# Kernel tuning notes

Measured on AMD Instinct MI355X. Metric: run time of the kernel, lower is better.

## Reference

```python
import jax, jax.numpy as jnp
import numpy as np

B, N_AIM, N_DET, C = 4, 2048, 2048, 256  # inplanes=256, inter_channels=128


def _lin(x, w, b):
    # torch nn.Linear: y = x @ W^T + b, weight shape [out, in]
    return jnp.einsum('bnc,dc->bnd', x, w) + b


def setup_inputs() -> dict:
    key = jax.random.key(0)
    ks = jax.random.split(key, 16)
    s = 1.0 / np.sqrt(C)
    inp = {
        'detect': jax.random.normal(ks[0], (B, N_DET, C), jnp.float32),
        'aim': jax.random.normal(ks[1], (B, N_AIM, C), jnp.float32),
    }
    names = ['g', 'g2', 'theta', 'phi', 'W', 'Q']
    for i, nm in enumerate(names):
        inp[nm + '_w'] = jax.random.uniform(ks[2 + 2 * i], (C, C), jnp.float32, -s, s)
        inp[nm + '_b'] = jax.random.uniform(ks[3 + 2 * i], (C,), jnp.float32, -s, s)
    return inp


def reference(detect, aim, g_w, g_b, g2_w, g2_b, theta_w, theta_b, phi_w, phi_b, W_w, W_b, Q_w, Q_b):
    b, na, c = aim.shape
    nd = detect.shape[1]
    ic = c // 2  # inter_channels

    # view(B, ic, -1) on a contiguous [B, N, C] tensor -> row-major reshape to [B, ic, 2N]
    d_x = _lin(detect, g_w, g_b).reshape(b, ic, -1).transpose(0, 2, 1)      # (B, 2Nd, ic)
    a_x = _lin(aim, g2_w, g2_b).reshape(b, ic, -1).transpose(0, 2, 1)       # (B, 2Na, ic)
    theta_x = _lin(aim, theta_w, theta_b).reshape(b, ic, -1).transpose(0, 2, 1)  # (B, 2Na, ic)
    phi_x = _lin(detect, phi_w, phi_b).reshape(b, ic, -1)                   # (B, ic, 2Nd)

    f = jnp.matmul(theta_x, phi_x)                 # (B, 2Na, 2Nd)
    f_div_C = f / f.shape[-1]                      # scale by 2*Nd
    fi_div_C = jnp.swapaxes(f, 1, 2) / f.shape[-2] # (B, 2Nd, 2Na), scale by 2*Na

    non_aim = jnp.matmul(f_div_C, d_x)             # (B, 2Na, ic)
    non_aim = non_aim.transpose(0, 2, 1).reshape(b, na, c)
    non_aim = _lin(non_aim, W_w, W_b) + aim

    non_det = jnp.matmul(fi_div_C, a_x)            # (B, 2Nd, ic)
    non_det = non_det.transpose(0, 2, 1).reshape(b, nd, c)
    non_det = _lin(non_det, Q_w, Q_b) + detect

    return (non_det, non_aim)
```

## Files before the change

kernel.cpp:

```cpp
#include <hip/hip_runtime.h>


typedef __attribute__((ext_vector_type(4))) float  f32x4;
typedef __attribute__((ext_vector_type(8))) __bf16 bf16x8;
typedef __attribute__((ext_vector_type(8))) unsigned short u16x8;
typedef __attribute__((ext_vector_type(4))) unsigned short u16x4;

__device__ inline unsigned short f2bf(float f) {
    union { float f; unsigned u; } c; c.f = f;
    unsigned r = c.u + 0x7FFF + ((c.u >> 16) & 1);
    return (unsigned short)(r >> 16);
}
__device__ inline bf16x8 ldfrag(const unsigned short* p) {
    return __builtin_bit_cast(bf16x8, *(const u16x8*)p);
}

__global__ __launch_bounds__(256)
void prep_kernel(const float* __restrict__ g_w, const float* __restrict__ g2_w,
                 const float* __restrict__ th_w, const float* __restrict__ ph_w,
                 const float* __restrict__ W_w, const float* __restrict__ Q_w,
                 const float* __restrict__ aim, const float* __restrict__ detect,
                 unsigned short* __restrict__ dst)
{
    const int z = blockIdx.y;
    const float* src; size_t n4; unsigned short* o;
    if (z == 0)      { src = g_w;    n4 = 16384;  o = dst; }
    else if (z == 1) { src = g2_w;   n4 = 16384;  o = dst + 65536; }
    else if (z == 2) { src = th_w;   n4 = 16384;  o = dst + 2 * 65536; }
    else if (z == 3) { src = ph_w;   n4 = 16384;  o = dst + 3 * 65536; }
    else if (z == 4) { src = W_w;    n4 = 16384;  o = dst + 4 * 65536; }
    else if (z == 5) { src = Q_w;    n4 = 16384;  o = dst + 5 * 65536; }
    else if (z == 6) { src = aim;    n4 = 524288; o = dst + 6 * 65536; }
    else             { src = detect; n4 = 524288; o = dst + 6 * 65536 + 2097152; }
    const size_t stride = (size_t)gridDim.x * 256;
    for (size_t i = blockIdx.x * 256 + threadIdx.x; i < n4; i += stride) {
        float4 v = ((const float4*)src)[i];
        u16x4 p; p[0]=f2bf(v.x); p[1]=f2bf(v.y); p[2]=f2bf(v.z); p[3]=f2bf(v.w);
        ((u16x4*)o)[i] = p;
    }
}

__global__ __launch_bounds__(256)
void lin4_kernel(const unsigned short* __restrict__ Abf, const unsigned short* __restrict__ Dbf,
                 const unsigned short* __restrict__ Wb,
                 const float* __restrict__ b_g, const float* __restrict__ b_g2,
                 const float* __restrict__ b_th, const float* __restrict__ b_ph,
                 unsigned short* __restrict__ T,  unsigned short* __restrict__ Ga,
                 unsigned short* __restrict__ P,  unsigned short* __restrict__ Gd)
{
    const int z = blockIdx.z, set = blockIdx.x;
    const unsigned short* A = z ? Dbf : Abf;
    const int wslot = z ? (set ? 0 : 3) : (set ? 1 : 2);
    const unsigned short* Wm = Wb + (size_t)wslot * 65536;
    const float* Bv = z ? (set ? b_g : b_ph) : (set ? b_g2 : b_th);
    unsigned short* O = z ? (set ? Gd : P) : (set ? Ga : T);
    const int m0 = blockIdx.y * 64;

    __shared__ unsigned short As[64][40];
    __shared__ unsigned short Bs[256][40];

    const int tid = threadIdx.x, lane = tid & 63, w = tid >> 6;
    const int wr = w >> 1, wc = w & 1, q = lane >> 4, ln = lane & 15;

    f32x4 acc[2][8] = {};

    for (int k0 = 0; k0 < 256; k0 += 32) {
        {
            int row = tid >> 2, c8 = tid & 3;
            *(u16x8*)&As[row][c8 * 8] = *(const u16x8*)(A + (size_t)(m0 + row) * 256 + k0 + c8 * 8);
        }
        #pragma unroll
        for (int i = 0; i < 4; ++i) {
            int c = tid + i * 256, row = c >> 2, c8 = c & 3;
            *(u16x8*)&Bs[row][c8 * 8] = *(const u16x8*)(Wm + (size_t)row * 256 + k0 + c8 * 8);
        }
        __syncthreads();
        bf16x8 af[2], bb[8];
        #pragma unroll
        for (int i = 0; i < 2; ++i) af[i] = ldfrag(&As[wr * 32 + i * 16 + ln][q * 8]);
        #pragma unroll
        for (int j = 0; j < 8; ++j) bb[j] = ldfrag(&Bs[wc * 128 + j * 16 + ln][q * 8]);
        #pragma unroll
        for (int i = 0; i < 2; ++i)
            #pragma unroll
            for (int j = 0; j < 8; ++j)
                acc[i][j] = __builtin_amdgcn_mfma_f32_16x16x32_bf16(af[i], bb[j], acc[i][j], 0, 0, 0);
        __syncthreads();
    }

    #pragma unroll
    for (int i = 0; i < 2; ++i)
        #pragma unroll
        for (int j = 0; j < 8; ++j) {
            int n = wc * 128 + j * 16 + ln;
            float bias = Bv[n];
            #pragma unroll
            for (int r = 0; r < 4; ++r) {
                int m = m0 + wr * 32 + i * 16 + q * 4 + r;
                O[(size_t)m * 256 + n] = f2bf(acc[i][j][r] + bias);
            }
        }
}

__global__ __launch_bounds__(256)
void s_part_kernel(const unsigned short* __restrict__ Gd, const unsigned short* __restrict__ P,
                   const unsigned short* __restrict__ Ga, const unsigned short* __restrict__ T,
                   float* __restrict__ Spart)
{
    const int bz = blockIdx.x;
    const int which = bz >> 7, rem = bz & 127, batch = rem >> 5, chunk = rem & 31;
    const unsigned short* A = (which ? Ga : Gd) + (size_t)batch * 524288;
    const unsigned short* B = (which ? T  : P ) + (size_t)batch * 524288;
    float* out = Spart + ((size_t)(which * 4 + batch) * 32 + chunk) * 16384;
    const int kbeg = chunk * 128;

    __shared__ unsigned short As[128][72], Bs[128][72];
    const int tid = threadIdx.x, lane = tid & 63, w = tid >> 6;
    const int wr = w >> 1, wc = w & 1, q = lane >> 4, ln = lane & 15;

    f32x4 acc[4][4] = {};

    for (int kk = 0; kk < 2; ++kk) {
        const int k0 = kbeg + kk * 64;
        #pragma unroll
        for (int i = 0; i < 4; ++i) {
            int c = tid + i * 256, row = c >> 3, c8 = c & 7;
            *(u16x8*)&As[row][c8 * 8] = *(const u16x8*)(A + (size_t)row * 4096 + k0 + c8 * 8);
            *(u16x8*)&Bs[row][c8 * 8] = *(const u16x8*)(B + (size_t)row * 4096 + k0 + c8 * 8);
        }
        __syncthreads();
        #pragma unroll
        for (int ks = 0; ks < 2; ++ks) {
            bf16x8 af[4], bb[4];
            #pragma unroll
            for (int i = 0; i < 4; ++i) af[i] = ldfrag(&As[wr * 64 + i * 16 + ln][ks * 32 + q * 8]);
            #pragma unroll
            for (int j = 0; j < 4; ++j) bb[j] = ldfrag(&Bs[wc * 64 + j * 16 + ln][ks * 32 + q * 8]);
            #pragma unroll
            for (int i = 0; i < 4; ++i)
                #pragma unroll
                for (int j = 0; j < 4; ++j)
                    acc[i][j] = __builtin_amdgcn_mfma_f32_16x16x32_bf16(af[i], bb[j], acc[i][j], 0, 0, 0);
        }
        __syncthreads();
    }

    #pragma unroll
    for (int i = 0; i < 4; ++i)
        #pragma unroll
        for (int j = 0; j < 4; ++j)
            #pragma unroll
            for (int r = 0; r < 4; ++r) {
                int m = wr * 64 + i * 16 + q * 4 + r, n = wc * 64 + j * 16 + ln;
                out[m * 128 + n] = acc[i][j][r];
            }
}

__global__ __launch_bounds__(256)
void sred_kernel(const float* __restrict__ Spart, float* __restrict__ S)
{
    const int idx = blockIdx.x * 256 + threadIdx.x;
    const int c = idx >> 14, e = idx & 16383;
    float s = 0.f;
    #pragma unroll
    for (int k = 0; k < 32; ++k) s += Spart[((size_t)(c * 32 + k) << 14) + e];
    S[idx] = s;
}

__global__ __launch_bounds__(256)
void nand_kernel(const float* __restrict__ S,
                 const unsigned short* __restrict__ T, const unsigned short* __restrict__ P,
                 unsigned short* __restrict__ NA, unsigned short* __restrict__ ND)
{
    const int which = blockIdx.z >> 2, batch = blockIdx.z & 3;
    const float* Sm = S + (size_t)(which * 4 + batch) * 16384;
    const unsigned short* Bsrc = (which ? P : T) + (size_t)batch * 524288;
    unsigned short* O = (which ? ND : NA) + (size_t)batch * 524288;
    const int j0 = blockIdx.x * 64;

    __shared__ unsigned short As[128][136];
    __shared__ unsigned short Bs[64][136];

    const int tid = threadIdx.x, lane = tid & 63, w = tid >> 6;
    const int wr = w >> 1, wc = w & 1, q = lane >> 4, ln = lane & 15;

    #pragma unroll
    for (int i = 0; i < 16; ++i) {
        int c = tid + i * 256, row = c >> 5, c4 = c & 31;
        float4 v = *((const float4*)(Sm + (size_t)row * 128) + c4);
        u16x4 p; p[0]=f2bf(v.x); p[1]=f2bf(v.y); p[2]=f2bf(v.z); p[3]=f2bf(v.w);
        *(u16x4*)&As[row][c4 * 4] = p;
    }
    #pragma unroll
    for (int i = 0; i < 4; ++i) {
        int c = tid + i * 256, k = c >> 3, jj0 = (c & 7) * 8;
        u16x8 v = *(const u16x8*)(Bsrc + (size_t)k * 4096 + j0 + jj0);
        #pragma unroll
        for (int jj = 0; jj < 8; ++jj) Bs[jj0 + jj][k] = v[jj];
    }
    __syncthreads();

    f32x4 acc[4][2] = {};
    #pragma unroll
    for (int ks = 0; ks < 4; ++ks) {
        bf16x8 af[4], bb[2];
        #pragma unroll
        for (int i = 0; i < 4; ++i) af[i] = ldfrag(&As[wr * 64 + i * 16 + ln][ks * 32 + q * 8]);
        #pragma unroll
        for (int j = 0; j < 2; ++j) bb[j] = ldfrag(&Bs[wc * 32 + j * 16 + ln][ks * 32 + q * 8]);
        #pragma unroll
        for (int i = 0; i < 4; ++i)
            #pragma unroll
            for (int j = 0; j < 2; ++j)
                acc[i][j] = __builtin_amdgcn_mfma_f32_16x16x32_bf16(af[i], bb[j], acc[i][j], 0, 0, 0);
    }

    #pragma unroll
    for (int i = 0; i < 4; ++i)
        #pragma unroll
        for (int j = 0; j < 2; ++j)
            #pragma unroll
            for (int r = 0; r < 4; ++r) {
                int m = wr * 64 + i * 16 + q * 4 + r;
                int jj = j0 + wc * 32 + j * 16 + ln;
                O[(size_t)m * 4096 + jj] = f2bf(acc[i][j][r] * (1.0f / 4096.0f));
            }
}

__global__ __launch_bounds__(256)
void final_kernel(const unsigned short* __restrict__ NA, const unsigned short* __restrict__ ND,
                  const unsigned short* __restrict__ Wb,
                  const float* __restrict__ W_b, const float* __restrict__ Q_b,
                  const float* __restrict__ aim, const float* __restrict__ detect,
                  float* __restrict__ out_aim, float* __restrict__ out_det)
{
    const int z = blockIdx.z;
    const unsigned short* A = z ? ND : NA;
    const unsigned short* Wm = Wb + (size_t)(z ? 5 : 4) * 65536;
    const float* Bv = z ? Q_b : W_b;
    const float* R  = z ? detect : aim;
    float* O = z ? out_det : out_aim;
    const int m0 = blockIdx.y * 64, n0 = blockIdx.x * 128;

    __shared__ unsigned short As[64][40], Bs[128][40];
    const int tid = threadIdx.x, lane = tid & 63, w = tid >> 6;
    const int wr = w >> 1, wc = w & 1, q = lane >> 4, ln = lane & 15;

    f32x4 acc[2][4] = {};

    for (int k0 = 0; k0 < 256; k0 += 32) {
        {
            int row = tid >> 2, c8 = tid & 3;
            *(u16x8*)&As[row][c8 * 8] = *(const u16x8*)(A + (size_t)(m0 + row) * 256 + k0 + c8 * 8);
        }
        #pragma unroll
        for (int i = 0; i < 2; ++i) {
            int c = tid + i * 256, row = c >> 2, c8 = c & 3;
            *(u16x8*)&Bs[row][c8 * 8] = *(const u16x8*)(Wm + (size_t)(n0 + row) * 256 + k0 + c8 * 8);
        }
        __syncthreads();
        bf16x8 af[2], bb[4];
        #pragma unroll
        for (int i = 0; i < 2; ++i) af[i] = ldfrag(&As[wr * 32 + i * 16 + ln][q * 8]);
        #pragma unroll
        for (int j = 0; j < 4; ++j) bb[j] = ldfrag(&Bs[wc * 64 + j * 16 + ln][q * 8]);
        #pragma unroll
        for (int i = 0; i < 2; ++i)
            #pragma unroll
            for (int j = 0; j < 4; ++j)
                acc[i][j] = __builtin_amdgcn_mfma_f32_16x16x32_bf16(af[i], bb[j], acc[i][j], 0, 0, 0);
        __syncthreads();
    }

    #pragma unroll
    for (int i = 0; i < 2; ++i)
        #pragma unroll
        for (int j = 0; j < 4; ++j) {
            int n = n0 + wc * 64 + j * 16 + ln;
            float bias = Bv[n];
            #pragma unroll
            for (int r = 0; r < 4; ++r) {
                int m = m0 + wr * 32 + i * 16 + q * 4 + r;
                O[(size_t)m * 256 + n] = acc[i][j][r] + bias + R[(size_t)m * 256 + n];
            }
        }
}

extern "C" void kernel_launch(void* const* d_in, const int* in_sizes, int n_in,
                              void* d_out, int out_size, void* d_ws, size_t ws_size,
                              hipStream_t stream)
{
    const float* detect = (const float*)d_in[0];
    const float* aim    = (const float*)d_in[1];
    const float* g_w  = (const float*)d_in[2];  const float* g_b  = (const float*)d_in[3];
    const float* g2_w = (const float*)d_in[4];  const float* g2_b = (const float*)d_in[5];
    const float* th_w = (const float*)d_in[6];  const float* th_b = (const float*)d_in[7];
    const float* ph_w = (const float*)d_in[8];  const float* ph_b = (const float*)d_in[9];
    const float* W_w  = (const float*)d_in[10]; const float* W_b  = (const float*)d_in[11];
    const float* Q_w  = (const float*)d_in[12]; const float* Q_b  = (const float*)d_in[13];

    const size_t TOT = 8192L * 256;

    unsigned short* ws16 = (unsigned short*)d_ws;
    unsigned short* Wbf = ws16;
    unsigned short* Abf = Wbf + 6 * 65536;
    unsigned short* Dbf = Abf + TOT;
    unsigned short* T   = Dbf + TOT;
    unsigned short* P   = T  + TOT;
    unsigned short* Gd  = P  + TOT;
    unsigned short* Ga  = Gd + TOT;
    unsigned short* NA  = Ga + TOT;
    unsigned short* ND  = NA + TOT;
    float* S     = (float*)(ND + TOT);
    float* Spart = S + 2 * 4 * 16384;

    float* out_det = (float*)d_out;
    float* out_aim = out_det + TOT;

    prep_kernel<<<dim3(256, 8), 256, 0, stream>>>(
        g_w, g2_w, th_w, ph_w, W_w, Q_w, aim, detect, Wbf);
    lin4_kernel<<<dim3(2, 128, 2), 256, 0, stream>>>(
        Abf, Dbf, Wbf, g_b, g2_b, th_b, ph_b, T, Ga, P, Gd);
    s_part_kernel<<<dim3(256), 256, 0, stream>>>(Gd, P, Ga, T, Spart);
    sred_kernel<<<dim3(512), 256, 0, stream>>>(Spart, S);
    nand_kernel<<<dim3(64, 1, 8), 256, 0, stream>>>(S, T, P, NA, ND);
    final_kernel<<<dim3(2, 128, 2), 256, 0, stream>>>(
        NA, ND, Wbf, W_b, Q_b, aim, detect, out_aim, out_det);
}
```

Baseline: 137.9 us.

## Fuse all stages into one cooperative persistent kernel with grid syncs

```diff
diff --git a/kernel.cpp b/kernel.cpp
--- a/kernel.cpp
+++ b/kernel.cpp
@@ -1,4 +1,7 @@
 #include <hip/hip_runtime.h>
+#include <hip/hip_cooperative_groups.h>
+
+namespace cg = cooperative_groups;
 
 
 typedef __attribute__((ext_vector_type(4))) float  f32x4;
@@ -15,55 +18,294 @@
     return __builtin_bit_cast(bf16x8, *(const u16x8*)p);
 }
 
+struct Params {
+    const float *detect, *aim;
+    const float *g_w, *g2_w, *th_w, *ph_w, *W_w, *Q_w;
+    const float *g_b, *g2_b, *th_b, *ph_b, *W_b, *Q_b;
+    unsigned short *Wbf, *Abf, *Dbf, *T, *P, *Gd, *Ga, *NA, *ND;
+    float *S, *Spart;
+    float *out_det, *out_aim;
+};
+
+__global__ __launch_bounds__(256, 2)
+void mega_kernel(Params p)
+{
+    cg::grid_group grid = cg::this_grid();
+    const int bx = blockIdx.x, tid = threadIdx.x;
+    const int lane = tid & 63, w = tid >> 6;
+    const int wr = w >> 1, wc = w & 1, q = lane >> 4, ln = lane & 15;
+
+    __shared__ union {
+        struct { unsigned short As[64][40];  unsigned short Bs[256][40]; } lin;
+        struct { unsigned short As[128][40]; unsigned short Bs[128][40]; } sp;
+        struct { unsigned short As[128][72]; unsigned short Bs[64][72];  } nd;
+        struct { unsigned short As[64][40];  unsigned short Bs[128][40]; } fin;
+    } sm;
+
+    {
+        const int z = bx >> 6, sub = bx & 63;
+        const float* src; size_t n4; unsigned short* o;
+        switch (z) {
+            case 0: src = p.g_w;    n4 = 16384;  o = p.Wbf;             break;
+            case 1: src = p.g2_w;   n4 = 16384;  o = p.Wbf + 65536;     break;
+            case 2: src = p.th_w;   n4 = 16384;  o = p.Wbf + 2*65536;   break;
+            case 3: src = p.ph_w;   n4 = 16384;  o = p.Wbf + 3*65536;   break;
+            case 4: src = p.W_w;    n4 = 16384;  o = p.Wbf + 4*65536;   break;
+            case 5: src = p.Q_w;    n4 = 16384;  o = p.Wbf + 5*65536;   break;
+            case 6: src = p.aim;    n4 = 524288; o = p.Abf;             break;
+            default:src = p.detect; n4 = 524288; o = p.Dbf;             break;
+        }
+        for (size_t i = (size_t)sub * 256 + tid; i < n4; i += 64 * 256) {
+            float4 v = ((const float4*)src)[i];
+            u16x4 pk; pk[0]=f2bf(v.x); pk[1]=f2bf(v.y); pk[2]=f2bf(v.z); pk[3]=f2bf(v.w);
+            ((u16x4*)o)[i] = pk;
+        }
+    }
+    grid.sync();
+
+    {
+        const int set = bx & 1, z = (bx >> 1) & 1;
+        const int m0 = (bx >> 2) * 64;
+        const unsigned short* A = z ? p.Dbf : p.Abf;
+        const int wslot = z ? (set ? 0 : 3) : (set ? 1 : 2);
+        const unsigned short* Wm = p.Wbf + (size_t)wslot * 65536;
+        const float* Bv = z ? (set ? p.g_b : p.ph_b) : (set ? p.g2_b : p.th_b);
+        unsigned short* O = z ? (set ? p.Gd : p.P) : (set ? p.Ga : p.T);
+
+        f32x4 acc[2][8] = {};
+        for (int k0 = 0; k0 < 256; k0 += 32) {
+            {
+                int row = tid >> 2, c8 = tid & 3;
+                *(u16x8*)&sm.lin.As[row][c8 * 8] =
+                    *(const u16x8*)(A + (size_t)(m0 + row) * 256 + k0 + c8 * 8);
+            }
+            #pragma unroll
+            for (int i = 0; i < 4; ++i) {
+                int c = tid + i * 256, row = c >> 2, c8 = c & 3;
+                *(u16x8*)&sm.lin.Bs[row][c8 * 8] =
+                    *(const u16x8*)(Wm + (size_t)row * 256 + k0 + c8 * 8);
+            }
+            __syncthreads();
+            bf16x8 af[2], bb[8];
+            #pragma unroll
+            for (int i = 0; i < 2; ++i) af[i] = ldfrag(&sm.lin.As[wr * 32 + i * 16 + ln][q * 8]);
+            #pragma unroll
+            for (int j = 0; j < 8; ++j) bb[j] = ldfrag(&sm.lin.Bs[wc * 128 + j * 16 + ln][q * 8]);
+            #pragma unroll
+            for (int i = 0; i < 2; ++i)
+                #pragma unroll
+                for (int j = 0; j < 8; ++j)
+                    acc[i][j] = __builtin_amdgcn_mfma_f32_16x16x32_bf16(af[i], bb[j], acc[i][j], 0, 0, 0);
+            __syncthreads();
+        }
+        #pragma unroll
+        for (int i = 0; i < 2; ++i)
+            #pragma unroll
+            for (int j = 0; j < 8; ++j) {
+                int n = wc * 128 + j * 16 + ln;
+                float bias = Bv[n];
+                #pragma unroll
+                for (int r = 0; r < 4; ++r) {
+                    int m = m0 + wr * 32 + i * 16 + q * 4 + r;
+                    O[(size_t)m * 256 + n] = f2bf(acc[i][j][r] + bias);
+                }
+            }
+    }
+    grid.sync();
+
+    if (bx < 256) {
+        const int which = bx >> 7, rem = bx & 127, batch = rem >> 5, chunk = rem & 31;
+        const unsigned short* A = (which ? p.Ga : p.Gd) + (size_t)batch * 524288;
+        const unsigned short* B = (which ? p.T  : p.P ) + (size_t)batch * 524288;
+        float* out = p.Spart + ((size_t)(which * 4 + batch) * 32 + chunk) * 16384;
+        const int kbeg = chunk * 128;
+
+        f32x4 acc[4][4] = {};
+        for (int k0 = kbeg; k0 < kbeg + 128; k0 += 32) {
+            #pragma unroll
+            for (int i = 0; i < 2; ++i) {
+                int c = tid + i * 256, row = c >> 2, c8 = c & 3;
+                *(u16x8*)&sm.sp.As[row][c8 * 8] = *(const u16x8*)(A + (size_t)row * 4096 + k0 + c8 * 8);
+                *(u16x8*)&sm.sp.Bs[row][c8 * 8] = *(const u16x8*)(B + (size_t)row * 4096 + k0 + c8 * 8);
+            }
+            __syncthreads();
+            bf16x8 af[4], bb[4];
+            #pragma unroll
+            for (int i = 0; i < 4; ++i) af[i] = ldfrag(&sm.sp.As[wr * 64 + i * 16 + ln][q * 8]);
+            #pragma unroll
+            for (int j = 0; j < 4; ++j) bb[j] = ldfrag(&sm.sp.Bs[wc * 64 + j * 16 + ln][q * 8]);
+            #pragma unroll
+            for (int i = 0; i < 4; ++i)
+                #pragma unroll
+                for (int j = 0; j < 4; ++j)
+                    acc[i][j] = __builtin_amdgcn_mfma_f32_16x16x32_bf16(af[i], bb[j], acc[i][j], 0, 0, 0);
+            __syncthreads();
+        }
+        #pragma unroll
+        for (int i = 0; i < 4; ++i)
+            #pragma unroll
+            for (int j = 0; j < 4; ++j)
+                #pragma unroll
+                for (int r = 0; r < 4; ++r) {
+                    int m = wr * 64 + i * 16 + q * 4 + r, n = wc * 64 + j * 16 + ln;
+                    out[m * 128 + n] = acc[i][j][r];
+                }
+    }
+    grid.sync();
+
+    {
+        const int idx = bx * 256 + tid;
+        const int c = idx >> 14, e = idx & 16383;
+        float s = 0.f;
+        #pragma unroll
+        for (int k = 0; k < 32; ++k) s += p.Spart[((size_t)(c * 32 + k) << 14) + e];
+        p.S[idx] = s;
+    }
+    grid.sync();
+
+    {
+        const int wb = bx >> 6, which = wb >> 2, batch = wb & 3;
+        const int j0 = (bx & 63) * 64;
+        const float* Sm = p.S + (size_t)(which * 4 + batch) * 16384;
+        const unsigned short* Bsrc = (which ? p.P : p.T) + (size_t)batch * 524288;
+        unsigned short* O = (which ? p.ND : p.NA) + (size_t)batch * 524288;
+
+        f32x4 acc[4][2] = {};
+        for (int h = 0; h < 2; ++h) {
+            const int k0 = h * 64;
+            #pragma unroll
+            for (int i = 0; i < 8; ++i) {
+                int c = tid + i * 256, row = c >> 4, c4 = c & 15;
+                float4 v = *((const float4*)(Sm + (size_t)row * 128 + k0) + c4);
+                u16x4 pk; pk[0]=f2bf(v.x); pk[1]=f2bf(v.y); pk[2]=f2bf(v.z); pk[3]=f2bf(v.w);
+                *(u16x4*)&sm.nd.As[row][c4 * 4] = pk;
+            }
+            #pragma unroll
+            for (int i = 0; i < 2; ++i) {
+                int c = tid + i * 256, k = c >> 3, jj0 = (c & 7) * 8;
+                u16x8 v = *(const u16x8*)(Bsrc + (size_t)(k0 + k) * 4096 + j0 + jj0);
+                #pragma unroll
+                for (int jj = 0; jj < 8; ++jj) sm.nd.Bs[jj0 + jj][k] = v[jj];
+            }
+            __syncthreads();
+            #pragma unroll
+            for (int ks = 0; ks < 2; ++ks) {
+                bf16x8 af[4], bb[2];
+                #pragma unroll
+                for (int i = 0; i < 4; ++i) af[i] = ldfrag(&sm.nd.As[wr * 64 + i * 16 + ln][ks * 32 + q * 8]);
+                #pragma unroll
+                for (int j = 0; j < 2; ++j) bb[j] = ldfrag(&sm.nd.Bs[wc * 32 + j * 16 + ln][ks * 32 + q * 8]);
+                #pragma unroll
+                for (int i = 0; i < 4; ++i)
+                    #pragma unroll
+                    for (int j = 0; j < 2; ++j)
+                        acc[i][j] = __builtin_amdgcn_mfma_f32_16x16x32_bf16(af[i], bb[j], acc[i][j], 0, 0, 0);
+            }
+            __syncthreads();
+        }
+        #pragma unroll
+        for (int i = 0; i < 4; ++i)
+            #pragma unroll
+            for (int j = 0; j < 2; ++j)
+                #pragma unroll
+                for (int r = 0; r < 4; ++r) {
+                    int m = wr * 64 + i * 16 + q * 4 + r;
+                    int jj = j0 + wc * 32 + j * 16 + ln;
+                    O[(size_t)m * 4096 + jj] = f2bf(acc[i][j][r] * (1.0f / 4096.0f));
+                }
+    }
+    grid.sync();
+
+    {
+        const int z = bx >> 8;
+        const int n0 = (bx & 1) * 128, m0 = ((bx >> 1) & 127) * 64;
+        const unsigned short* A = z ? p.ND : p.NA;
+        const unsigned short* Wm = p.Wbf + (size_t)(z ? 5 : 4) * 65536;
+        const float* Bv = z ? p.Q_b : p.W_b;
+        const float* R  = z ? p.detect : p.aim;
+        float* O = z ? p.out_det : p.out_aim;
+
+        f32x4 acc[2][4] = {};
+        for (int k0 = 0; k0 < 256; k0 += 32) {
+            {
+                int row = tid >> 2, c8 = tid & 3;
+                *(u16x8*)&sm.fin.As[row][c8 * 8] =
+                    *(const u16x8*)(A + (size_t)(m0 + row) * 256 + k0 + c8 * 8);
+            }
+            #pragma unroll
+            for (int i = 0; i < 2; ++i) {
+                int c = tid + i * 256, row = c >> 2, c8 = c & 3;
+                *(u16x8*)&sm.fin.Bs[row][c8 * 8] =
+                    *(const u16x8*)(Wm + (size_t)(n0 + row) * 256 + k0 + c8 * 8);
+            }
+            __syncthreads();
+            bf16x8 af[2], bb[4];
+            #pragma unroll
+            for (int i = 0; i < 2; ++i) af[i] = ldfrag(&sm.fin.As[wr * 32 + i * 16 + ln][q * 8]);
+            #pragma unroll
+            for (int j = 0; j < 4; ++j) bb[j] = ldfrag(&sm.fin.Bs[wc * 64 + j * 16 + ln][q * 8]);
+            #pragma unroll
+            for (int i = 0; i < 2; ++i)
+                #pragma unroll
+                for (int j = 0; j < 4; ++j)
+                    acc[i][j] = __builtin_amdgcn_mfma_f32_16x16x32_bf16(af[i], bb[j], acc[i][j], 0, 0, 0);
+            __syncthreads();
+        }
+        #pragma unroll
+        for (int i = 0; i < 2; ++i)
+            #pragma unroll
+            for (int j = 0; j < 4; ++j) {
+                int n = n0 + wc * 64 + j * 16 + ln;
+                float bias = Bv[n];
+                #pragma unroll
+                for (int r = 0; r < 4; ++r) {
+                    int m = m0 + wr * 32 + i * 16 + q * 4 + r;
+                    O[(size_t)m * 256 + n] = acc[i][j][r] + bias + R[(size_t)m * 256 + n];
+                }
+            }
+    }
+}
+
 __global__ __launch_bounds__(256)
-void prep_kernel(const float* __restrict__ g_w, const float* __restrict__ g2_w,
-                 const float* __restrict__ th_w, const float* __restrict__ ph_w,
-                 const float* __restrict__ W_w, const float* __restrict__ Q_w,
-                 const float* __restrict__ aim, const float* __restrict__ detect,
-                 unsigned short* __restrict__ dst)
+void prep_kernel(Params p)
 {
     const int z = blockIdx.y;
     const float* src; size_t n4; unsigned short* o;
-    if (z == 0)      { src = g_w;    n4 = 16384;  o = dst; }
-    else if (z == 1) { src = g2_w;   n4 = 16384;  o = dst + 65536; }
-    else if (z == 2) { src = th_w;   n4 = 16384;  o = dst + 2 * 65536; }
-    else if (z == 3) { src = ph_w;   n4 = 16384;  o = dst + 3 * 65536; }
-    else if (z == 4) { src = W_w;    n4 = 16384;  o = dst + 4 * 65536; }
-    else if (z == 5) { src = Q_w;    n4 = 16384;  o = dst + 5 * 65536; }
-    else if (z == 6) { src = aim;    n4 = 524288; o = dst + 6 * 65536; }
-    else             { src = detect; n4 = 524288; o = dst + 6 * 65536 + 2097152; }
+    switch (z) {
+        case 0: src = p.g_w;    n4 = 16384;  o = p.Wbf;             break;
+        case 1: src = p.g2_w;   n4 = 16384;  o = p.Wbf + 65536;     break;
+        case 2: src = p.th_w;   n4 = 16384;  o = p.Wbf + 2*65536;   break;
+        case 3: src = p.ph_w;   n4 = 16384;  o = p.Wbf + 3*65536;   break;
+        case 4: src = p.W_w;    n4 = 16384;  o = p.Wbf + 4*65536;   break;
+        case 5: src = p.Q_w;    n4 = 16384;  o = p.Wbf + 5*65536;   break;
+        case 6: src = p.aim;    n4 = 524288; o = p.Abf;             break;
+        default:src = p.detect; n4 = 524288; o = p.Dbf;             break;
+    }
     const size_t stride = (size_t)gridDim.x * 256;
     for (size_t i = blockIdx.x * 256 + threadIdx.x; i < n4; i += stride) {
         float4 v = ((const float4*)src)[i];
-        u16x4 p; p[0]=f2bf(v.x); p[1]=f2bf(v.y); p[2]=f2bf(v.z); p[3]=f2bf(v.w);
-        ((u16x4*)o)[i] = p;
+        u16x4 pk; pk[0]=f2bf(v.x); pk[1]=f2bf(v.y); pk[2]=f2bf(v.z); pk[3]=f2bf(v.w);
+        ((u16x4*)o)[i] = pk;
     }
 }
 
 __global__ __launch_bounds__(256)
-void lin4_kernel(const unsigned short* __restrict__ Abf, const unsigned short* __restrict__ Dbf,
-                 const unsigned short* __restrict__ Wb,
-                 const float* __restrict__ b_g, const float* __restrict__ b_g2,
-                 const float* __restrict__ b_th, const float* __restrict__ b_ph,
-                 unsigned short* __restrict__ T,  unsigned short* __restrict__ Ga,
-                 unsigned short* __restrict__ P,  unsigned short* __restrict__ Gd)
+void lin4_kernel(Params p)
 {
     const int z = blockIdx.z, set = blockIdx.x;
-    const unsigned short* A = z ? Dbf : Abf;
+    const unsigned short* A = z ? p.Dbf : p.Abf;
     const int wslot = z ? (set ? 0 : 3) : (set ? 1 : 2);
-    const unsigned short* Wm = Wb + (size_t)wslot * 65536;
-    const float* Bv = z ? (set ? b_g : b_ph) : (set ? b_g2 : b_th);
-    unsigned short* O = z ? (set ? Gd : P) : (set ? Ga : T);
+    const unsigned short* Wm = p.Wbf + (size_t)wslot * 65536;
+    const float* Bv = z ? (set ? p.g_b : p.ph_b) : (set ? p.g2_b : p.th_b);
+    unsigned short* O = z ? (set ? p.Gd : p.P) : (set ? p.Ga : p.T);
     const int m0 = blockIdx.y * 64;
 
     __shared__ unsigned short As[64][40];
     __shared__ unsigned short Bs[256][40];
-
     const int tid = threadIdx.x, lane = tid & 63, w = tid >> 6;
     const int wr = w >> 1, wc = w & 1, q = lane >> 4, ln = lane & 15;
 
     f32x4 acc[2][8] = {};
-
     for (int k0 = 0; k0 < 256; k0 += 32) {
         {
             int row = tid >> 2, c8 = tid & 3;
@@ -87,7 +329,6 @@
                 acc[i][j] = __builtin_amdgcn_mfma_f32_16x16x32_bf16(af[i], bb[j], acc[i][j], 0, 0, 0);
         __syncthreads();
     }
-
     #pragma unroll
     for (int i = 0; i < 2; ++i)
         #pragma unroll
@@ -103,15 +344,13 @@
 }
 
 __global__ __launch_bounds__(256)
-void s_part_kernel(const unsigned short* __restrict__ Gd, const unsigned short* __restrict__ P,
-                   const unsigned short* __restrict__ Ga, const unsigned short* __restrict__ T,
-                   float* __restrict__ Spart)
+void s_part_kernel(Params p)
 {
     const int bz = blockIdx.x;
     const int which = bz >> 7, rem = bz & 127, batch = rem >> 5, chunk = rem & 31;
-    const unsigned short* A = (which ? Ga : Gd) + (size_t)batch * 524288;
-    const unsigned short* B = (which ? T  : P ) + (size_t)batch * 524288;
-    float* out = Spart + ((size_t)(which * 4 + batch) * 32 + chunk) * 16384;
+    const unsigned short* A = (which ? p.Ga : p.Gd) + (size_t)batch * 524288;
+    const unsigned short* B = (which ? p.T  : p.P ) + (size_t)batch * 524288;
+    float* out = p.Spart + ((size_t)(which * 4 + batch) * 32 + chunk) * 16384;
     const int kbeg = chunk * 128;
 
     __shared__ unsigned short As[128][72], Bs[128][72];
@@ -119,7 +358,6 @@
     const int wr = w >> 1, wc = w & 1, q = lane >> 4, ln = lane & 15;
 
     f32x4 acc[4][4] = {};
-
     for (int kk = 0; kk < 2; ++kk) {
         const int k0 = kbeg + kk * 64;
         #pragma unroll
@@ -144,7 +382,6 @@
         }
         __syncthreads();
     }
-
     #pragma unroll
     for (int i = 0; i < 4; ++i)
         #pragma unroll
@@ -157,30 +394,27 @@
 }
 
 __global__ __launch_bounds__(256)
-void sred_kernel(const float* __restrict__ Spart, float* __restrict__ S)
+void sred_kernel(Params p)
 {
     const int idx = blockIdx.x * 256 + threadIdx.x;
     const int c = idx >> 14, e = idx & 16383;
     float s = 0.f;
     #pragma unroll
-    for (int k = 0; k < 32; ++k) s += Spart[((size_t)(c * 32 + k) << 14) + e];
-    S[idx] = s;
+    for (int k = 0; k < 32; ++k) s += p.Spart[((size_t)(c * 32 + k) << 14) + e];
+    p.S[idx] = s;
 }
 
 __global__ __launch_bounds__(256)
-void nand_kernel(const float* __restrict__ S,
-                 const unsigned short* __restrict__ T, const unsigned short* __restrict__ P,
-                 unsigned short* __restrict__ NA, unsigned short* __restrict__ ND)
+void nand_kernel(Params p)
 {
     const int which = blockIdx.z >> 2, batch = blockIdx.z & 3;
-    const float* Sm = S + (size_t)(which * 4 + batch) * 16384;
-    const unsigned short* Bsrc = (which ? P : T) + (size_t)batch * 524288;
-    unsigned short* O = (which ? ND : NA) + (size_t)batch * 524288;
+    const float* Sm = p.S + (size_t)(which * 4 + batch) * 16384;
+    const unsigned short* Bsrc = (which ? p.P : p.T) + (size_t)batch * 524288;
+    unsigned short* O = (which ? p.ND : p.NA) + (size_t)batch * 524288;
     const int j0 = blockIdx.x * 64;
 
     __shared__ unsigned short As[128][136];
     __shared__ unsigned short Bs[64][136];
-
     const int tid = threadIdx.x, lane = tid & 63, w = tid >> 6;
     const int wr = w >> 1, wc = w & 1, q = lane >> 4, ln = lane & 15;
 
@@ -188,8 +422,8 @@
     for (int i = 0; i < 16; ++i) {
         int c = tid + i * 256, row = c >> 5, c4 = c & 31;
         float4 v = *((const float4*)(Sm + (size_t)row * 128) + c4);
-        u16x4 p; p[0]=f2bf(v.x); p[1]=f2bf(v.y); p[2]=f2bf(v.z); p[3]=f2bf(v.w);
-        *(u16x4*)&As[row][c4 * 4] = p;
+        u16x4 pk; pk[0]=f2bf(v.x); pk[1]=f2bf(v.y); pk[2]=f2bf(v.z); pk[3]=f2bf(v.w);
+        *(u16x4*)&As[row][c4 * 4] = pk;
     }
     #pragma unroll
     for (int i = 0; i < 4; ++i) {
@@ -214,7 +448,6 @@
             for (int j = 0; j < 2; ++j)
                 acc[i][j] = __builtin_amdgcn_mfma_f32_16x16x32_bf16(af[i], bb[j], acc[i][j], 0, 0, 0);
     }
-
     #pragma unroll
     for (int i = 0; i < 4; ++i)
         #pragma unroll
@@ -228,18 +461,14 @@
 }
 
 __global__ __launch_bounds__(256)
-void final_kernel(const unsigned short* __restrict__ NA, const unsigned short* __restrict__ ND,
-                  const unsigned short* __restrict__ Wb,
-                  const float* __restrict__ W_b, const float* __restrict__ Q_b,
-                  const float* __restrict__ aim, const float* __restrict__ detect,
-                  float* __restrict__ out_aim, float* __restrict__ out_det)
+void final_kernel(Params p)
 {
     const int z = blockIdx.z;
-    const unsigned short* A = z ? ND : NA;
-    const unsigned short* Wm = Wb + (size_t)(z ? 5 : 4) * 65536;
-    const float* Bv = z ? Q_b : W_b;
-    const float* R  = z ? detect : aim;
-    float* O = z ? out_det : out_aim;
+    const unsigned short* A = z ? p.ND : p.NA;
+    const unsigned short* Wm = p.Wbf + (size_t)(z ? 5 : 4) * 65536;
+    const float* Bv = z ? p.Q_b : p.W_b;
+    const float* R  = z ? p.detect : p.aim;
+    float* O = z ? p.out_det : p.out_aim;
     const int m0 = blockIdx.y * 64, n0 = blockIdx.x * 128;
 
     __shared__ unsigned short As[64][40], Bs[128][40];
@@ -247,7 +476,6 @@
     const int wr = w >> 1, wc = w & 1, q = lane >> 4, ln = lane & 15;
 
     f32x4 acc[2][4] = {};
-
     for (int k0 = 0; k0 < 256; k0 += 32) {
         {
             int row = tid >> 2, c8 = tid & 3;
@@ -271,7 +499,6 @@
                 acc[i][j] = __builtin_amdgcn_mfma_f32_16x16x32_bf16(af[i], bb[j], acc[i][j], 0, 0, 0);
         __syncthreads();
     }
-
     #pragma unroll
     for (int i = 0; i < 2; ++i)
         #pragma unroll
@@ -290,40 +517,43 @@
                               void* d_out, int out_size, void* d_ws, size_t ws_size,
                               hipStream_t stream)
 {
-    const float* detect = (const float*)d_in[0];
-    const float* aim    = (const float*)d_in[1];
-    const float* g_w  = (const float*)d_in[2];  const float* g_b  = (const float*)d_in[3];
-    const float* g2_w = (const float*)d_in[4];  const float* g2_b = (const float*)d_in[5];
-    const float* th_w = (const float*)d_in[6];  const float* th_b = (const float*)d_in[7];
-    const float* ph_w = (const float*)d_in[8];  const float* ph_b = (const float*)d_in[9];
-    const float* W_w  = (const float*)d_in[10]; const float* W_b  = (const float*)d_in[11];
-    const float* Q_w  = (const float*)d_in[12]; const float* Q_b  = (const float*)d_in[13];
+    Params p;
+    p.detect = (const float*)d_in[0];
+    p.aim    = (const float*)d_in[1];
+    p.g_w  = (const float*)d_in[2];  p.g_b  = (const float*)d_in[3];
+    p.g2_w = (const float*)d_in[4];  p.g2_b = (const float*)d_in[5];
+    p.th_w = (const float*)d_in[6];  p.th_b = (const float*)d_in[7];
+    p.ph_w = (const float*)d_in[8];  p.ph_b = (const float*)d_in[9];
+    p.W_w  = (const float*)d_in[10]; p.W_b  = (const float*)d_in[11];
+    p.Q_w  = (const float*)d_in[12]; p.Q_b  = (const float*)d_in[13];
 
     const size_t TOT = 8192L * 256;
 
     unsigned short* ws16 = (unsigned short*)d_ws;
-    unsigned short* Wbf = ws16;
-    unsigned short* Abf = Wbf + 6 * 65536;
-    unsigned short* Dbf = Abf + TOT;
-    unsigned short* T   = Dbf + TOT;
-    unsigned short* P   = T  + TOT;
-    unsigned short* Gd  = P  + TOT;
-    unsigned short* Ga  = Gd + TOT;
-    unsigned short* NA  = Ga + TOT;
-    unsigned short* ND  = NA + TOT;
-    float* S     = (float*)(ND + TOT);
-    float* Spart = S + 2 * 4 * 16384;
-
-    float* out_det = (float*)d_out;
-    float* out_aim = out_det + TOT;
-
-    prep_kernel<<<dim3(256, 8), 256, 0, stream>>>(
-        g_w, g2_w, th_w, ph_w, W_w, Q_w, aim, detect, Wbf);
-    lin4_kernel<<<dim3(2, 128, 2), 256, 0, stream>>>(
-        Abf, Dbf, Wbf, g_b, g2_b, th_b, ph_b, T, Ga, P, Gd);
-    s_part_kernel<<<dim3(256), 256, 0, stream>>>(Gd, P, Ga, T, Spart);
-    sred_kernel<<<dim3(512), 256, 0, stream>>>(Spart, S);
-    nand_kernel<<<dim3(64, 1, 8), 256, 0, stream>>>(S, T, P, NA, ND);
-    final_kernel<<<dim3(2, 128, 2), 256, 0, stream>>>(
-        NA, ND, Wbf, W_b, Q_b, aim, detect, out_aim, out_det);
-}
+    p.Wbf = ws16;
+    p.Abf = p.Wbf + 6 * 65536;
+    p.Dbf = p.Abf + TOT;
+    p.T   = p.Dbf + TOT;
+    p.P   = p.T  + TOT;
+    p.Gd  = p.P  + TOT;
+    p.Ga  = p.Gd + TOT;
+    p.NA  = p.Ga + TOT;
+    p.ND  = p.NA + TOT;
+    p.S     = (float*)(p.ND + TOT);
+    p.Spart = p.S + 2 * 4 * 16384;
+
+    p.out_det = (float*)d_out;
+    p.out_aim = p.out_det + TOT;
+
+    void* args[] = { &p };
+    hipError_t e = hipLaunchCooperativeKernel((const void*)mega_kernel, dim3(512),
+                                              dim3(256), args, 0, stream);
+    if (e != hipSuccess) {
+        prep_kernel<<<dim3(256, 8), 256, 0, stream>>>(p);
+        lin4_kernel<<<dim3(2, 128, 2), 256, 0, stream>>>(p);
+        s_part_kernel<<<dim3(256), 256, 0, stream>>>(p);
+        sred_kernel<<<dim3(512), 256, 0, stream>>>(p);
+        nand_kernel<<<dim3(64, 1, 8), 256, 0, stream>>>(p);
+        final_kernel<<<dim3(2, 128, 2), 256, 0, stream>>>(p);
+    }
+}
```

New measurement: 467.7 us. 3.39x slower.
